# Kernel tuning notes

Measured on AMD Instinct MI355X. Metric: run time of the kernel, lower is better.

Reference implementation:

```python
import jax, jax.numpy as jnp
import numpy as np

GROUP_SIZE = 64  # init_kwargs: group_size
BATCH = 1024
NEURONS = 65536  # must be divisible by GROUP_SIZE


def setup_inputs() -> dict:
    key = jax.random.key(0)
    kx, kp = jax.random.split(key)
    # positive activations (firing rates) so group sums are nonzero
    x = jax.random.uniform(kx, (BATCH, NEURONS), dtype=jnp.float32)
    # build()'s np.random.shuffle(np.arange(neuron_num)) -> fixed random permutation
    index = jax.random.permutation(kp, jnp.arange(NEURONS, dtype=jnp.int32))
    return {"x": x, "index": index}


def reference(x, index):
    # x: [B, N] activations; index: [N] permutation defining group membership.
    # Group g = permuted neurons [g*GROUP_SIZE, (g+1)*GROUP_SIZE).
    B, N = x.shape
    gathered = x[:, index].reshape(B, N // GROUP_SIZE, GROUP_SIZE)  # [B, G, gs]
    norm = gathered / jnp.sum(gathered, axis=-1, keepdims=True)     # divisive normalization
    # scatter back to original neuron positions: out[:, index] = norm
    out = jnp.zeros_like(x).at[:, index].set(norm.reshape(B, N))
    return out
```

## Files before the change

kernel.cpp:

```cpp
#include <hip/hip_runtime.h>
#include <hip/hip_bf16.h>

#define BATCH   1024
#define NEUR    65536
#define NGRP    1024
#define NCHUNK  8
#define CHUNK   (NEUR / NCHUNK)
#define CHUNK_F4 (CHUNK / 4)
#define BLK1    512
#define F4T1    (CHUNK_F4 / BLK1)
#define KMAX    16
#define SENT    CHUNK
#define BLK     1024
#define ROW_F4  (NEUR / 4)
#define HALF_F4 (ROW_F4 / 2)
#define H_ITERS (HALF_F4 / BLK)
#define BUCKET_ELEMS (NCHUNK * NGRP * KMAX)
#define SPILL_CAP 1024

typedef float          f32x4 __attribute__((ext_vector_type(4)));
typedef unsigned short u16x8 __attribute__((ext_vector_type(8)));
typedef unsigned short u16x4 __attribute__((ext_vector_type(4)));


__global__ void build_tables(const int* __restrict__ index,
                             unsigned short* __restrict__ gof,
                             unsigned short* __restrict__ bucket,
                             unsigned int* __restrict__ spill) {
    const int p    = blockIdx.x * blockDim.x + threadIdx.x;
    const int lane = threadIdx.x & 63;
    const int g    = p >> 6;
    const int s    = index[p];
    gof[s] = (unsigned short)g;
    const int c = s >> 13;
    unsigned long long mc = 0;
    int count[NCHUNK];
    #pragma unroll
    for (int cc = 0; cc < NCHUNK; ++cc) {
        unsigned long long m = __ballot(c == cc);
        if (cc == c) mc = m;
        count[cc] = __popcll(m);
    }
    const int k = __popcll(mc & ((1ull << lane) - 1ull));
    if (k < KMAX) {
        bucket[((size_t)(c * NGRP + g)) * KMAX + k] = (unsigned short)(s & (CHUNK - 1));
    } else {
        unsigned int pos = atomicAdd(spill, 1u);
        if (pos < SPILL_CAP - 1)
            spill[1 + pos] = ((unsigned)g << 16) | (unsigned)s;
    }
    #pragma unroll
    for (int j = 0; j < 2; ++j) {
        const int slot = lane + j * 64;
        const int cc = slot >> 4, kk = slot & 15;
        if (kk >= count[cc])
            bucket[((size_t)(cc * NGRP + g)) * KMAX + kk] = (unsigned short)SENT;
    }
}

__global__ __launch_bounds__(BLK1, 8)
void k1_partial(const float* __restrict__ x,
                const unsigned short* __restrict__ bucket,
                const unsigned int* __restrict__ spill,
                float* __restrict__ part) {
    __shared__ float xs[CHUNK + 16];
    const int bc = blockIdx.x;
    const int b  = bc >> 3;
    const int c  = bc & 7;
    const int t  = threadIdx.x;

    const unsigned short* __restrict__ bk0 =
        bucket + ((size_t)(c * NGRP + t)) * KMAX;
    const unsigned short* __restrict__ bk1 =
        bucket + ((size_t)(c * NGRP + t + 512)) * KMAX;
    const u16x8 w0 = *(const u16x8*)(bk0);
    const u16x8 w1 = *(const u16x8*)(bk0 + 8);
    const u16x8 w2 = *(const u16x8*)(bk1);
    const u16x8 w3 = *(const u16x8*)(bk1 + 8);
    const unsigned int ns = spill[0];

    if (t == 0) xs[SENT] = 0.0f;

    const float4* __restrict__ src =
        (const float4*)(x + (size_t)b * NEUR + (size_t)c * CHUNK);
    float4* xs4 = (float4*)xs;
    #pragma unroll
    for (int i = 0; i < F4T1; ++i) {
        __builtin_amdgcn_global_load_lds(
            (const __attribute__((address_space(1))) unsigned int*)(src + i * BLK1 + t),
            (__attribute__((address_space(3))) unsigned int*)(xs4 + i * BLK1 + t),
            16, 0, 0);
    }
    __syncthreads();

    float a0 = 0.0f, a1 = 0.0f, b0 = 0.0f, b1 = 0.0f;
    #pragma unroll
    for (int j = 0; j < 8; ++j) {
        a0 += xs[w0[j]];
        a1 += xs[w1[j]];
        b0 += xs[w2[j]];
        b1 += xs[w3[j]];
    }

    for (unsigned int e = 0; e < ns; ++e) {
        const unsigned int ent = spill[1 + e];
        if (((ent >> 13) & 7u) == (unsigned)c) {
            const float v = xs[ent & 0x1FFFu];
            const int gg = (int)(ent >> 16);
            if (gg == t)            a1 += v;
            else if (gg == t + 512) b1 += v;
        }
    }

    float* __restrict__ prow = part + ((size_t)b * NCHUNK + c) * NGRP;
    prow[t]       = a0 + a1;
    prow[t + 512] = b0 + b1;
}

__global__ __launch_bounds__(BLK, 8)
void k3_scale(const float* __restrict__ x,
              const unsigned short* __restrict__ gof,
              const float* __restrict__ part,
              float* __restrict__ out) {
    __shared__ float rsum[NGRP];
    const int rb   = blockIdx.x;
    const int b    = (BATCH - 1) - (rb >> 1);
    const int half = rb & 1;
    const int t    = threadIdx.x;

    const float* __restrict__ prow = part + (size_t)b * NCHUNK * NGRP;
    float s = 0.0f;
    #pragma unroll
    for (int c = 0; c < NCHUNK; ++c) s += prow[c * NGRP + t];
    rsum[t] = 1.0f / s;
    __syncthreads();

    const float4* __restrict__ xrow4 = (const float4*)(x + (size_t)b * NEUR);
    const u16x4*  __restrict__ gof4  = (const u16x4*)gof;
    f32x4*        __restrict__ orow4 = (f32x4*)(out + (size_t)b * NEUR);

    #pragma unroll
    for (int it = 0; it < H_ITERS; ++it) {
        const int e = half * HALF_F4 + it * BLK + t;
        const float4 v = xrow4[e];
        const u16x4 g = gof4[e];
        f32x4 o;
        o.x = v.x * rsum[g.x];
        o.y = v.y * rsum[g.y];
        o.z = v.z * rsum[g.z];
        o.w = v.w * rsum[g.w];
        __builtin_nontemporal_store(o, &orow4[e]);
    }
}

extern "C" void kernel_launch(void* const* d_in, const int* in_sizes, int n_in,
                              void* d_out, int out_size, void* d_ws, size_t ws_size,
                              hipStream_t stream) {
    const float* x     = (const float*)d_in[0];
    const int*   index = (const int*)d_in[1];
    float*       out   = (float*)d_out;

    unsigned short* gof    = (unsigned short*)d_ws;
    unsigned short* bucket = gof + NEUR;
    float*          part   = (float*)(bucket + BUCKET_ELEMS);
    unsigned int*   spill  = (unsigned int*)(part + (size_t)BATCH * NCHUNK * NGRP);

    hipMemsetAsync(spill, 0, sizeof(unsigned int), stream);
    build_tables<<<NEUR / BLK, BLK, 0, stream>>>(index, gof, bucket, spill);
    k1_partial<<<BATCH * NCHUNK, BLK1, 0, stream>>>(x, bucket, spill, part);
    k3_scale<<<BATCH * 2, BLK, 0, stream>>>(x, gof, part, out);
}
```

Baseline: 147.2 us.

## Split spill list per chunk and halve scale kernel block size

```diff
diff --git a/kernel.cpp b/kernel.cpp
--- a/kernel.cpp
+++ b/kernel.cpp
@@ -12,11 +12,12 @@
 #define KMAX    16
 #define SENT    CHUNK
 #define BLK     1024
+#define BLK3    512
 #define ROW_F4  (NEUR / 4)
 #define HALF_F4 (ROW_F4 / 2)
-#define H_ITERS (HALF_F4 / BLK)
+#define H_ITERS (HALF_F4 / BLK3)
 #define BUCKET_ELEMS (NCHUNK * NGRP * KMAX)
-#define SPILL_CAP 1024
+#define SPILL_PER_C 120
 
 typedef float          f32x4 __attribute__((ext_vector_type(4)));
 typedef unsigned short u16x8 __attribute__((ext_vector_type(8)));
@@ -45,9 +46,9 @@
     if (k < KMAX) {
         bucket[((size_t)(c * NGRP + g)) * KMAX + k] = (unsigned short)(s & (CHUNK - 1));
     } else {
-        unsigned int pos = atomicAdd(spill, 1u);
-        if (pos < SPILL_CAP - 1)
-            spill[1 + pos] = ((unsigned)g << 16) | (unsigned)s;
+        unsigned int pos = atomicAdd(&spill[c], 1u);
+        if (pos < SPILL_PER_C)
+            spill[NCHUNK + c * SPILL_PER_C + pos] = ((unsigned)g << 16) | (unsigned)s;
     }
     #pragma unroll
     for (int j = 0; j < 2; ++j) {
@@ -77,7 +78,7 @@
     const u16x8 w1 = *(const u16x8*)(bk0 + 8);
     const u16x8 w2 = *(const u16x8*)(bk1);
     const u16x8 w3 = *(const u16x8*)(bk1 + 8);
-    const unsigned int ns = spill[0];
+    const unsigned int ns = spill[c];
 
     if (t == 0) xs[SENT] = 0.0f;
 
@@ -102,14 +103,13 @@
         b1 += xs[w3[j]];
     }
 
+    const unsigned int* __restrict__ sl = spill + NCHUNK + c * SPILL_PER_C;
     for (unsigned int e = 0; e < ns; ++e) {
-        const unsigned int ent = spill[1 + e];
-        if (((ent >> 13) & 7u) == (unsigned)c) {
-            const float v = xs[ent & 0x1FFFu];
-            const int gg = (int)(ent >> 16);
-            if (gg == t)            a1 += v;
-            else if (gg == t + 512) b1 += v;
-        }
+        const unsigned int ent = sl[e];
+        const float v = xs[ent & 0x1FFFu];
+        const int gg = (int)(ent >> 16);
+        if (gg == t)            a1 += v;
+        else if (gg == t + 512) b1 += v;
     }
 
     float* __restrict__ prow = part + ((size_t)b * NCHUNK + c) * NGRP;
@@ -117,7 +117,7 @@
     prow[t + 512] = b0 + b1;
 }
 
-__global__ __launch_bounds__(BLK, 8)
+__global__ __launch_bounds__(BLK3, 8)
 void k3_scale(const float* __restrict__ x,
               const unsigned short* __restrict__ gof,
               const float* __restrict__ part,
@@ -129,19 +129,23 @@
     const int t    = threadIdx.x;
 
     const float* __restrict__ prow = part + (size_t)b * NCHUNK * NGRP;
-    float s = 0.0f;
+    float s0 = 0.0f, s1 = 0.0f;
     #pragma unroll
-    for (int c = 0; c < NCHUNK; ++c) s += prow[c * NGRP + t];
-    rsum[t] = 1.0f / s;
+    for (int c = 0; c < NCHUNK; ++c) {
+        s0 += prow[c * NGRP + t];
+        s1 += prow[c * NGRP + t + 512];
+    }
+    rsum[t]       = 1.0f / s0;
+    rsum[t + 512] = 1.0f / s1;
     __syncthreads();
 
     const float4* __restrict__ xrow4 = (const float4*)(x + (size_t)b * NEUR);
     const u16x4*  __restrict__ gof4  = (const u16x4*)gof;
     f32x4*        __restrict__ orow4 = (f32x4*)(out + (size_t)b * NEUR);
 
-    #pragma unroll
+    #pragma unroll 4
     for (int it = 0; it < H_ITERS; ++it) {
-        const int e = half * HALF_F4 + it * BLK + t;
+        const int e = half * HALF_F4 + it * BLK3 + t;
         const float4 v = xrow4[e];
         const u16x4 g = gof4[e];
         f32x4 o;
@@ -149,7 +153,7 @@
         o.y = v.y * rsum[g.y];
         o.z = v.z * rsum[g.z];
         o.w = v.w * rsum[g.w];
-        __builtin_nontemporal_store(o, &orow4[e]);
+        orow4[e] = o;
     }
 }
 
@@ -165,8 +169,8 @@
     float*          part   = (float*)(bucket + BUCKET_ELEMS);
     unsigned int*   spill  = (unsigned int*)(part + (size_t)BATCH * NCHUNK * NGRP);
 
-    hipMemsetAsync(spill, 0, sizeof(unsigned int), stream);
+    hipMemsetAsync(spill, 0, NCHUNK * sizeof(unsigned int), stream);
     build_tables<<<NEUR / BLK, BLK, 0, stream>>>(index, gof, bucket, spill);
     k1_partial<<<BATCH * NCHUNK, BLK1, 0, stream>>>(x, bucket, spill, part);
-    k3_scale<<<BATCH * 2, BLK, 0, stream>>>(x, gof, part, out);
+    k3_scale<<<BATCH * 2, BLK3, 0, stream>>>(x, gof, part, out);
 }
```

Result: slower. 168.9 us (+14.7%).
